# Kernel tuning notes

Measured on AMD Instinct MI355X. Metric: run time of the kernel, lower is better.

The kernel has to match this reference:

```python
import jax, jax.numpy as jnp
import numpy as np

HEAD_SIZE = 64
N_EMBED = 1024
B, T = 8, 2048


def setup_inputs() -> dict:
    key = jax.random.key(0)
    ks = jax.random.split(key, 7)
    s = lambda fan_in: 1.0 / np.sqrt(fan_in)
    return {
        "x": jax.random.normal(ks[0], (B, T, N_EMBED), dtype=jnp.float32),
        # Linear weights stored as (in, out) so projection is x @ W + b
        "Wk": jax.random.uniform(ks[1], (N_EMBED, HEAD_SIZE), jnp.float32, -s(N_EMBED), s(N_EMBED)),
        "bk": jax.random.uniform(ks[2], (HEAD_SIZE,), jnp.float32, -s(N_EMBED), s(N_EMBED)),
        "Wq": jax.random.uniform(ks[3], (N_EMBED, HEAD_SIZE), jnp.float32, -s(N_EMBED), s(N_EMBED)),
        "bq": jax.random.uniform(ks[4], (HEAD_SIZE,), jnp.float32, -s(N_EMBED), s(N_EMBED)),
        "Wv": jax.random.uniform(ks[5], (N_EMBED, HEAD_SIZE), jnp.float32, -s(N_EMBED), s(N_EMBED)),
        "bv": jax.random.uniform(ks[6], (HEAD_SIZE,), jnp.float32, -s(N_EMBED), s(N_EMBED)),
    }


def reference(x, Wk, bk, Wq, bq, Wv, bv):
    Bb, Tt, C = x.shape
    k = x @ Wk + bk  # [B,T,H]
    q = x @ Wq + bq
    v = x @ Wv + bv
    # NOTE: original computes k @ q^T (keys as rows, queries as cols)
    wei = jnp.einsum("bth,bsh->bts", k, q) * (C ** -0.5)  # [B,T,T]
    causal = jnp.tril(jnp.ones((Tt, Tt), dtype=bool))
    wei = jnp.where(causal, wei, -jnp.inf)
    # softplus instead of softmax; softplus(-inf) = 0, stable via logaddexp
    wei = jnp.logaddexp(wei, 0.0)
    # dropout omitted (eval mode / deterministic reference)
    out = jnp.einsum("bts,bsh->bth", wei, v)  # [B,T,H]
    return out
```

## Files before the change

### kernel.cpp

```cpp
#include <hip/hip_runtime.h>
#include <hip/hip_bf16.h>
#include <stdint.h>

#define HEAD 64
#define CEMB 1024
#define BB 8
#define TSEQ 2048

typedef __attribute__((ext_vector_type(8))) short bf16x8;
typedef __attribute__((ext_vector_type(4))) float f32x4;

__device__ __forceinline__ unsigned short f2bf(float f) {
    union { float f; uint32_t u; } c; c.f = f;
    uint32_t u = c.u + 0x7FFF + ((c.u >> 16) & 1);
    return (unsigned short)(u >> 16);
}

__global__ __launch_bounds__(256) void prep_w(
        const float* __restrict__ Wk, const float* __restrict__ bk,
        const float* __restrict__ Wq, const float* __restrict__ bq,
        const float* __restrict__ Wv, const float* __restrict__ bv,
        unsigned short* __restrict__ WT, float* __restrict__ biasb) {
    int n = blockIdx.x;
    int proj = n >> 6, col = n & 63;
    const float* W  = (proj == 0) ? Wk : (proj == 1) ? Wq : Wv;
    const float* bi = (proj == 0) ? bk : (proj == 1) ? bq : bv;
    float scale = (proj == 1) ? 0.03125f : 1.0f;
    for (int k = threadIdx.x; k < CEMB; k += 256)
        WT[n * CEMB + k] = f2bf(W[k * HEAD + col] * scale);
    if (threadIdx.x == 0) biasb[n] = bi[col] * scale;
}

__global__ __launch_bounds__(512) void proj_gemm(
        const float* __restrict__ x, const unsigned short* __restrict__ WT,
        const float* __restrict__ biasb,
        unsigned short* __restrict__ Kb, unsigned short* __restrict__ Qb,
        unsigned short* __restrict__ VTb) {
    __shared__ __align__(16) unsigned short As[64 * 40];
    __shared__ __align__(16) unsigned short Bs[192 * 40];

    const int tid  = threadIdx.x;
    const int lane = tid & 63, w = tid >> 6;
    const int l15  = lane & 15, q4 = lane >> 4;
    const int mw   = w & 1, nw = w >> 1;
    const long rowbase = (long)blockIdx.x * 64;

    f32x4 z = {0.f, 0.f, 0.f, 0.f};
    f32x4 acc[2][3];
    for (int a = 0; a < 2; a++) for (int b = 0; b < 3; b++) acc[a][b] = z;

    const int ar  = tid >> 3;
    const int akq = tid & 7;
    const float* xg = x + (rowbase + ar) * CEMB + akq * 4;

    for (int k0 = 0; k0 < CEMB; k0 += 32) {
        float4 av = *(const float4*)(xg + k0);
        ushort4 a4;
        a4.x = f2bf(av.x); a4.y = f2bf(av.y); a4.z = f2bf(av.z); a4.w = f2bf(av.w);
        *(ushort4*)(&As[ar * 40 + akq * 4]) = a4;
        {
            int n = tid >> 2, kq = tid & 3;
            if (n < 192)
                *(int4*)(&Bs[n * 40 + kq * 8]) =
                    *(const int4*)(WT + (long)n * CEMB + k0 + kq * 8);
            if (tid < 256) {
                int n2 = 128 + (tid >> 2), kq2 = tid & 3;
                *(int4*)(&Bs[n2 * 40 + kq2 * 8]) =
                    *(const int4*)(WT + (long)n2 * CEMB + k0 + kq2 * 8);
            }
        }
        __syncthreads();
        bf16x8 afr[2], bfr[3];
        for (int mt = 0; mt < 2; mt++)
            afr[mt] = *(const bf16x8*)(&As[((mw * 2 + mt) * 16 + l15) * 40 + q4 * 8]);
        for (int j = 0; j < 3; j++)
            bfr[j] = *(const bf16x8*)(&Bs[((nw * 3 + j) * 16 + l15) * 40 + q4 * 8]);
        for (int mt = 0; mt < 2; mt++)
            for (int j = 0; j < 3; j++)
                acc[mt][j] = __builtin_amdgcn_mfma_f32_16x16x32_bf16(
                    afr[mt], bfr[j], acc[mt][j], 0, 0, 0);
        __syncthreads();
    }

    for (int j = 0; j < 3; j++) {
        int n = nw * 48 + j * 16 + l15;
        float bias = biasb[n];
        for (int mt = 0; mt < 2; mt++) {
            long row0 = rowbase + (mw * 2 + mt) * 16 + q4 * 4;
            if (n < 128) {
                unsigned short* dst = (n < 64) ? (Kb + row0 * HEAD + n)
                                               : (Qb + row0 * HEAD + (n - 64));
                for (int r = 0; r < 4; r++)
                    dst[r * HEAD] = f2bf(acc[mt][j][r] + bias);
            } else {
                int h = n - 128;
                long b = row0 >> 11; int t = (int)(row0 & 2047);
                ushort4 p;
                p.x = f2bf(acc[mt][j][0] + bias);
                p.y = f2bf(acc[mt][j][1] + bias);
                p.z = f2bf(acc[mt][j][2] + bias);
                p.w = f2bf(acc[mt][j][3] + bias);
                *(ushort4*)(VTb + b * (HEAD * (long)TSEQ) + (long)h * TSEQ + t) = p;
            }
        }
    }
}

__global__ __launch_bounds__(256) void attn(
        const unsigned short* __restrict__ Kb, const unsigned short* __restrict__ Qb,
        const unsigned short* __restrict__ VTb, float* __restrict__ out) {
    __shared__ __align__(16) unsigned short Pl[4][16 * 40];
    __shared__ __align__(16) float red[3][64 * 20];

    const int tid = threadIdx.x;
    const int lane = tid & 63, w = tid >> 6;
    const int l15 = lane & 15, q4 = lane >> 4;

    const int bid = blockIdx.x;
    const int ti = 127 - (bid >> 3);
    const int b = bid & 7;
    const int t0 = ti * 16;

    const unsigned short* kb  = Kb  + (long)b * TSEQ * HEAD;
    const unsigned short* qb  = Qb  + (long)b * TSEQ * HEAD;
    const unsigned short* vtb = VTb + (long)b * HEAD * TSEQ;

    bf16x8 kf0 = *(const bf16x8*)(kb + (t0 + l15) * HEAD + q4 * 8);
    bf16x8 kf1 = *(const bf16x8*)(kb + (t0 + l15) * HEAD + 32 + q4 * 8);

    f32x4 z = {0.f, 0.f, 0.f, 0.f};
    f32x4 oacc[4] = {z, z, z, z};

    unsigned short* myP = &Pl[w][0];
    const int nchunk = (t0 + 15) / 32 + 1;

    for (int c = w; c < nchunk; c += 4) {
        const int s0 = c * 32;
        f32x4 st[2];
        for (int tile = 0; tile < 2; tile++) {
            int sb = s0 + tile * 16;
            bf16x8 qf0 = *(const bf16x8*)(qb + (sb + l15) * HEAD + q4 * 8);
            bf16x8 qf1 = *(const bf16x8*)(qb + (sb + l15) * HEAD + 32 + q4 * 8);
            f32x4 sc = z;
            sc = __builtin_amdgcn_mfma_f32_16x16x32_bf16(qf0, kf0, sc, 0, 0, 0);
            sc = __builtin_amdgcn_mfma_f32_16x16x32_bf16(qf1, kf1, sc, 0, 0, 0);
            st[tile] = sc;
        }
        const int tg = t0 + l15;
        for (int tile = 0; tile < 2; tile++) {
            ushort4 pk;
            unsigned short pv[4];
            for (int r = 0; r < 4; r++) {
                int sg = s0 + tile * 16 + q4 * 4 + r;
                float p = __logf(1.0f + __expf(st[tile][r]));
                if (sg > tg) p = 0.0f;
                pv[r] = f2bf(p);
            }
            pk.x = pv[0]; pk.y = pv[1]; pk.z = pv[2]; pk.w = pv[3];
            *(ushort4*)(myP + l15 * 40 + tile * 16 + q4 * 4) = pk;
        }
        __threadfence_block();
        bf16x8 pf = *(const bf16x8*)(myP + l15 * 40 + q4 * 8);
        for (int hh = 0; hh < 4; hh++) {
            bf16x8 vf = *(const bf16x8*)(vtb + (hh * 16 + l15) * (long)TSEQ + s0 + q4 * 8);
            oacc[hh] = __builtin_amdgcn_mfma_f32_16x16x32_bf16(vf, pf, oacc[hh], 0, 0, 0);
        }
    }

    if (w > 0) {
        float* r0 = &red[w - 1][lane * 20];
        for (int hh = 0; hh < 4; hh++)
            *(f32x4*)(r0 + hh * 4) = oacc[hh];
    }
    __syncthreads();
    if (w == 0) {
        for (int i = 0; i < 3; i++) {
            const float* r0 = &red[i][lane * 20];
            for (int hh = 0; hh < 4; hh++)
                oacc[hh] += *(const f32x4*)(r0 + hh * 4);
        }
        float* ob = out + ((long)b * TSEQ + t0 + l15) * HEAD + q4 * 4;
        for (int hh = 0; hh < 4; hh++)
            *(f32x4*)(ob + hh * 16) = oacc[hh];
    }
}

extern "C" void kernel_launch(void* const* d_in, const int* in_sizes, int n_in,
                              void* d_out, int out_size, void* d_ws, size_t ws_size,
                              hipStream_t stream) {
    const float* x  = (const float*)d_in[0];
    const float* Wk = (const float*)d_in[1];
    const float* bk = (const float*)d_in[2];
    const float* Wq = (const float*)d_in[3];
    const float* bq = (const float*)d_in[4];
    const float* Wv = (const float*)d_in[5];
    const float* bv = (const float*)d_in[6];
    float* out = (float*)d_out;

    char* ws = (char*)d_ws;
    unsigned short* WT    = (unsigned short*)(ws);
    float*          biasb = (float*)(ws + 393216);
    unsigned short* Kb    = (unsigned short*)(ws + 524288);
    unsigned short* Qb    = (unsigned short*)(ws + 524288 + 2097152);
    unsigned short* VTb   = (unsigned short*)(ws + 524288 + 4194304);

    prep_w<<<192, 256, 0, stream>>>(Wk, bk, Wq, bq, Wv, bv, WT, biasb);
    proj_gemm<<<256, 512, 0, stream>>>(x, WT, biasb, Kb, Qb, VTb);
    attn<<<1024, 256, 0, stream>>>(Kb, Qb, VTb, out);
}
```

Baseline: 174.2 us.

## Pipeline projection GEMM with double-buffered weights and direct x register loads

The projection GEMM now uses 32-row tiles with 256 threads over 512 blocks. It loads x directly from global memory into registers as MFMA A-fragments, skipping the LDS staging for x. Weight tiles of 64 k-values are double-buffered in LDS, and the next x and weight segment is prefetched into registers during the current MFMAs, which halves the barriers and overlaps loads with compute. prep_w is rewritten to transpose the weights through shared memory with coalesced reads and vector writes. The trade-off is that each block rereads the whole weight matrix for fewer rows, and the kernel needs more registers for the prefetch.

```diff
diff --git a/kernel.cpp b/kernel.cpp
--- a/kernel.cpp
+++ b/kernel.cpp
@@ -6,6 +6,7 @@
 #define CEMB 1024
 #define BB 8
 #define TSEQ 2048
+#define PBK 64
 
 typedef __attribute__((ext_vector_type(8))) short bf16x8;
 typedef __attribute__((ext_vector_type(4))) float f32x4;
@@ -21,87 +22,115 @@
         const float* __restrict__ Wq, const float* __restrict__ bq,
         const float* __restrict__ Wv, const float* __restrict__ bv,
         unsigned short* __restrict__ WT, float* __restrict__ biasb) {
-    int n = blockIdx.x;
-    int proj = n >> 6, col = n & 63;
-    const float* W  = (proj == 0) ? Wk : (proj == 1) ? Wq : Wv;
-    const float* bi = (proj == 0) ? bk : (proj == 1) ? bq : bv;
-    float scale = (proj == 1) ? 0.03125f : 1.0f;
-    for (int k = threadIdx.x; k < CEMB; k += 256)
-        WT[n * CEMB + k] = f2bf(W[k * HEAD + col] * scale);
-    if (threadIdx.x == 0) biasb[n] = bi[col] * scale;
-}
-
-__global__ __launch_bounds__(512) void proj_gemm(
+    __shared__ float Ws[64][68];
+    const int p = blockIdx.x >> 4, kc = blockIdx.x & 15;
+    const float* W  = (p == 0) ? Wk : (p == 1) ? Wq : Wv;
+    const float* bi = (p == 0) ? bk : (p == 1) ? bq : bv;
+    const float scale = (p == 1) ? 0.03125f : 1.0f;
+    const int tid = threadIdx.x;
+    const int h4 = (tid & 15) * 4;
+    for (int r = 0; r < 4; r++) {
+        int kl = (tid >> 4) + r * 16;
+        float4 v = *(const float4*)(W + (long)(kc * 64 + kl) * 64 + h4);
+        *(float4*)(&Ws[kl][h4]) = v;
+    }
+    __syncthreads();
+    const int h = tid >> 2, k0 = (tid & 3) * 16;
+    unsigned short ov[16];
+    for (int i = 0; i < 16; i++) ov[i] = f2bf(Ws[k0 + i][h] * scale);
+    unsigned short* dst = WT + (long)(p * 64 + h) * CEMB + kc * 64 + k0;
+    *(int4*)(dst)     = *(int4*)(ov);
+    *(int4*)(dst + 8) = *((int4*)(ov) + 1);
+    if (kc == 0 && tid < 64) biasb[p * 64 + tid] = bi[tid] * scale;
+}
+
+__global__ __launch_bounds__(256) void proj_gemm(
         const float* __restrict__ x, const unsigned short* __restrict__ WT,
         const float* __restrict__ biasb,
         unsigned short* __restrict__ Kb, unsigned short* __restrict__ Qb,
         unsigned short* __restrict__ VTb) {
-    __shared__ __align__(16) unsigned short As[64 * 40];
-    __shared__ __align__(16) unsigned short Bs[192 * 40];
-
-    const int tid  = threadIdx.x;
+    __shared__ __align__(16) unsigned short Bs[2][192 * 72];
+
+    const int tid = threadIdx.x;
     const int lane = tid & 63, w = tid >> 6;
-    const int l15  = lane & 15, q4 = lane >> 4;
-    const int mw   = w & 1, nw = w >> 1;
-    const long rowbase = (long)blockIdx.x * 64;
+    const int l15 = lane & 15, q4 = lane >> 4;
+    const int mw = w & 1, nw = w >> 1;
+    const long rowbase = (long)blockIdx.x * 32;
+
+    const float* xg = x + (rowbase + mw * 16 + l15) * CEMB + q4 * 8;
 
     f32x4 z = {0.f, 0.f, 0.f, 0.f};
-    f32x4 acc[2][3];
-    for (int a = 0; a < 2; a++) for (int b = 0; b < 3; b++) acc[a][b] = z;
-
-    const int ar  = tid >> 3;
-    const int akq = tid & 7;
-    const float* xg = x + (rowbase + ar) * CEMB + akq * 4;
-
-    for (int k0 = 0; k0 < CEMB; k0 += 32) {
-        float4 av = *(const float4*)(xg + k0);
-        ushort4 a4;
-        a4.x = f2bf(av.x); a4.y = f2bf(av.y); a4.z = f2bf(av.z); a4.w = f2bf(av.w);
-        *(ushort4*)(&As[ar * 40 + akq * 4]) = a4;
-        {
-            int n = tid >> 2, kq = tid & 3;
-            if (n < 192)
-                *(int4*)(&Bs[n * 40 + kq * 8]) =
-                    *(const int4*)(WT + (long)n * CEMB + k0 + kq * 8);
-            if (tid < 256) {
-                int n2 = 128 + (tid >> 2), kq2 = tid & 3;
-                *(int4*)(&Bs[n2 * 40 + kq2 * 8]) =
-                    *(const int4*)(WT + (long)n2 * CEMB + k0 + kq2 * 8);
+    f32x4 acc[6];
+    for (int j = 0; j < 6; j++) acc[j] = z;
+
+    float4 apf[4];
+    int4   bpf[6];
+
+    for (int kk = 0; kk < 2; kk++)
+        for (int c = 0; c < 2; c++)
+            apf[kk * 2 + c] = *(const float4*)(xg + kk * 32 + c * 4);
+    for (int i = 0; i < 6; i++) {
+        int c = i * 256 + tid, n = c >> 3, kc = c & 7;
+        bpf[i] = *(const int4*)(WT + (long)n * CEMB + kc * 8);
+    }
+    for (int i = 0; i < 6; i++) {
+        int c = i * 256 + tid, n = c >> 3, kc = c & 7;
+        *(int4*)(&Bs[0][n * 72 + kc * 8]) = bpf[i];
+    }
+    __syncthreads();
+
+    for (int seg = 0; seg < 16; seg++) {
+        const int cur = seg & 1;
+        bf16x8 af[2];
+        for (int kk = 0; kk < 2; kk++) {
+            unsigned short t8[8];
+            const float* f = (const float*)&apf[kk * 2];
+            for (int e = 0; e < 8; e++) t8[e] = f2bf(f[e]);
+            af[kk] = *(bf16x8*)t8;
+        }
+        if (seg < 15) {
+            const float* xs = xg + (seg + 1) * PBK;
+            for (int kk = 0; kk < 2; kk++)
+                for (int c = 0; c < 2; c++)
+                    apf[kk * 2 + c] = *(const float4*)(xs + kk * 32 + c * 4);
+            for (int i = 0; i < 6; i++) {
+                int c = i * 256 + tid, n = c >> 3, kc = c & 7;
+                bpf[i] = *(const int4*)(WT + (long)n * CEMB + (seg + 1) * PBK + kc * 8);
+            }
+        }
+        for (int kk = 0; kk < 2; kk++)
+            for (int j = 0; j < 6; j++) {
+                bf16x8 bf = *(const bf16x8*)(
+                    &Bs[cur][(nw * 96 + j * 16 + l15) * 72 + kk * 32 + q4 * 8]);
+                acc[j] = __builtin_amdgcn_mfma_f32_16x16x32_bf16(af[kk], bf, acc[j], 0, 0, 0);
+            }
+        if (seg < 15) {
+            for (int i = 0; i < 6; i++) {
+                int c = i * 256 + tid, n = c >> 3, kc = c & 7;
+                *(int4*)(&Bs[cur ^ 1][n * 72 + kc * 8]) = bpf[i];
             }
         }
         __syncthreads();
-        bf16x8 afr[2], bfr[3];
-        for (int mt = 0; mt < 2; mt++)
-            afr[mt] = *(const bf16x8*)(&As[((mw * 2 + mt) * 16 + l15) * 40 + q4 * 8]);
-        for (int j = 0; j < 3; j++)
-            bfr[j] = *(const bf16x8*)(&Bs[((nw * 3 + j) * 16 + l15) * 40 + q4 * 8]);
-        for (int mt = 0; mt < 2; mt++)
-            for (int j = 0; j < 3; j++)
-                acc[mt][j] = __builtin_amdgcn_mfma_f32_16x16x32_bf16(
-                    afr[mt], bfr[j], acc[mt][j], 0, 0, 0);
-        __syncthreads();
-    }
-
-    for (int j = 0; j < 3; j++) {
-        int n = nw * 48 + j * 16 + l15;
-        float bias = biasb[n];
-        for (int mt = 0; mt < 2; mt++) {
-            long row0 = rowbase + (mw * 2 + mt) * 16 + q4 * 4;
-            if (n < 128) {
-                unsigned short* dst = (n < 64) ? (Kb + row0 * HEAD + n)
-                                               : (Qb + row0 * HEAD + (n - 64));
-                for (int r = 0; r < 4; r++)
-                    dst[r * HEAD] = f2bf(acc[mt][j][r] + bias);
-            } else {
-                int h = n - 128;
-                long b = row0 >> 11; int t = (int)(row0 & 2047);
-                ushort4 p;
-                p.x = f2bf(acc[mt][j][0] + bias);
-                p.y = f2bf(acc[mt][j][1] + bias);
-                p.z = f2bf(acc[mt][j][2] + bias);
-                p.w = f2bf(acc[mt][j][3] + bias);
-                *(ushort4*)(VTb + b * (HEAD * (long)TSEQ) + (long)h * TSEQ + t) = p;
-            }
+    }
+
+    for (int j = 0; j < 6; j++) {
+        const int n = nw * 96 + j * 16 + l15;
+        const float bias = biasb[n];
+        const long row0 = rowbase + mw * 16 + q4 * 4;
+        if (n < 128) {
+            unsigned short* dst = (n < 64) ? (Kb + row0 * HEAD + n)
+                                           : (Qb + row0 * HEAD + (n - 64));
+            for (int r = 0; r < 4; r++)
+                dst[r * HEAD] = f2bf(acc[j][r] + bias);
+        } else {
+            const int h = n - 128;
+            const long b = row0 >> 11; const int t = (int)(row0 & 2047);
+            ushort4 pk;
+            pk.x = f2bf(acc[j][0] + bias);
+            pk.y = f2bf(acc[j][1] + bias);
+            pk.z = f2bf(acc[j][2] + bias);
+            pk.w = f2bf(acc[j][3] + bias);
+            *(ushort4*)(VTb + b * (HEAD * (long)TSEQ) + (long)h * TSEQ + t) = pk;
         }
     }
 }
@@ -204,7 +233,7 @@
     unsigned short* Qb    = (unsigned short*)(ws + 524288 + 2097152);
     unsigned short* VTb   = (unsigned short*)(ws + 524288 + 4194304);
 
-    prep_w<<<192, 256, 0, stream>>>(Wk, bk, Wq, bq, Wv, bv, WT, biasb);
-    proj_gemm<<<256, 512, 0, stream>>>(x, WT, biasb, Kb, Qb, VTb);
+    prep_w<<<48, 256, 0, stream>>>(Wk, bk, Wq, bq, Wv, bv, WT, biasb);
+    proj_gemm<<<512, 256, 0, stream>>>(x, WT, biasb, Kb, Qb, VTb);
     attn<<<1024, 256, 0, stream>>>(Kb, Qb, VTb, out);
 }
```

Measured after the change: 163.9 us. 1.06x faster.
